# Optimization experiments

Measured on AMD Instinct MI355X. Metric: run time of the kernel, lower is better.

Reference implementation:

```python
import jax, jax.numpy as jnp
import numpy as np

D_MODEL = 1024
NUM_HEADS = 16
HEAD_DIM = D_MODEL // NUM_HEADS


def setup_inputs() -> dict:
    key = jax.random.key(0)
    k_x, k_wqkv, k_bqkv, k_wfc, k_bfc = jax.random.split(key, 5)
    scale_in = 1.0 / np.sqrt(D_MODEL)
    return {
        "x": jax.random.normal(k_x, (2, 2048, D_MODEL), dtype=jnp.float32),
        # torch nn.Linear stores weight as [out_features, in_features]
        "w_qkv": jax.random.uniform(k_wqkv, (3 * D_MODEL, D_MODEL), jnp.float32, -scale_in, scale_in),
        "b_qkv": jax.random.uniform(k_bqkv, (3 * D_MODEL,), jnp.float32, -scale_in, scale_in),
        "w_fc": jax.random.uniform(k_wfc, (D_MODEL, D_MODEL), jnp.float32, -scale_in, scale_in),
        "b_fc": jax.random.uniform(k_bfc, (D_MODEL,), jnp.float32, -scale_in, scale_in),
    }


def reference(x, w_qkv, b_qkv, w_fc, b_fc):
    B, S, _ = x.shape
    # fused QKV projection: [B,S,3*d_model]
    qkv = jnp.einsum("bsd,ed->bse", x, w_qkv) + b_qkv
    # [B,S,H,3*head_dim] -> [B,H,S,3*head_dim]
    qkv = qkv.reshape(B, S, NUM_HEADS, 3 * HEAD_DIM).transpose(0, 2, 1, 3)
    Q, K, V = jnp.split(qkv, 3, axis=-1)  # each [B,H,S,head_dim]
    scores = jnp.einsum("bhqd,bhkd->bhqk", Q, K) / np.sqrt(HEAD_DIM).astype(np.float32)
    attention = jax.nn.softmax(scores, axis=-1)  # [B,H,S,S]
    values = jnp.einsum("bhqk,bhkd->bhqd", attention, V)
    # [B,H,S,head_dim] -> [B,S,d_model]
    values = values.transpose(0, 2, 1, 3).reshape(B, S, D_MODEL)
    out = jnp.einsum("bsd,ed->bse", values, w_fc) + b_fc
    return out
```

## Files before the change

kernel.cpp:

```cpp
#include <hip/hip_runtime.h>
#include <hip/hip_bf16.h>
#include <hip/hip_fp16.h>

#define D_MODEL 1024
#define NH 16
#define HD 64
#define BATCH 2
#define SEQ 2048

typedef __attribute__((ext_vector_type(8))) short short8;
typedef __attribute__((ext_vector_type(4))) float floatx4;
typedef __attribute__((ext_vector_type(8))) _Float16 half8;

static __device__ __forceinline__ short f2bf(float f) {
    __hip_bfloat16 h = __float2bfloat16(f);
    return *reinterpret_cast<short*>(&h);
}
static __device__ __forceinline__ unsigned int pk2bf(float a, float b) {
    float2 t; t.x = a; t.y = b;
    __hip_bfloat162 h2 = __float22bfloat162_rn(t);
    return *reinterpret_cast<unsigned int*>(&h2);
}

#define GLDS(gp, lp) __builtin_amdgcn_global_load_lds( \
    (const __attribute__((address_space(1))) void*)(gp), \
    (__attribute__((address_space(3))) void*)(lp), 16, 0, 0)

__global__ __launch_bounds__(256) void cvt_all(
    const float* __restrict__ x, const float* __restrict__ wq,
    const float* __restrict__ wf,
    short* __restrict__ Xb, short* __restrict__ Wqb, short* __restrict__ Wfb)
{
    int i = blockIdx.x * 256 + threadIdx.x;
    const float* src; short* dst; int off;
    if (i < 524288)      { src = x;  dst = Xb;  off = i; }
    else if (i < 917504) { src = wq; dst = Wqb; off = i - 524288; }
    else                 { src = wf; dst = Wfb; off = i - 917504; }
    float4 a = *reinterpret_cast<const float4*>(src + off * 8);
    float4 b = *reinterpret_cast<const float4*>(src + off * 8 + 4);
    short8 o;
    o[0] = f2bf(a.x); o[1] = f2bf(a.y); o[2] = f2bf(a.z); o[3] = f2bf(a.w);
    o[4] = f2bf(b.x); o[5] = f2bf(b.y); o[6] = f2bf(b.z); o[7] = f2bf(b.w);
    *reinterpret_cast<short8*>(dst + off * 8) = o;
}

__global__ __launch_bounds__(256) void qkv_gemm(
    const short* __restrict__ X, const short* __restrict__ W,
    const float* __restrict__ bias,
    short* __restrict__ Qs, short* __restrict__ Ks, short* __restrict__ Vt_g)
{
    __shared__ __align__(16) short As[128 * 128];
    __shared__ __align__(16) short Bs[128 * 128];
    const int tid = threadIdx.x;

    const int lin = blockIdx.x;
    const int g = lin & 7;
    const int loc = lin >> 3;
    const int mi = loc / 3;
    const int j3 = loc - mi * 3;
    const int m0 = mi * 128;
    const int n0 = (g + 8 * j3) * 128;
    const int bi = m0 >> 11, sl0 = m0 & 2047;

    const int w = tid >> 6, lane = tid & 63;
    const int quad = lane >> 4, l15 = lane & 15;
    const int wm2 = w >> 1, wn2 = w & 1;

    const int rg = lane >> 3;
    const int sl = lane & 7;
    const int cg = sl ^ rg;

    floatx4 acc[4][4];
#pragma unroll
    for (int i = 0; i < 4; i++)
#pragma unroll
        for (int j = 0; j < 4; j++) acc[i][j] = (floatx4)0.0f;

    for (int k0 = 0; k0 < 1024; k0 += 128) {
        __syncthreads();
#pragma unroll
        for (int jj = 0; jj < 4; jj++) {
            int grp = w * 4 + jj;
            int r = grp * 8 + rg;
#pragma unroll
            for (int kh = 0; kh < 2; kh++) {
                GLDS(&X[(size_t)(m0 + r) * 1024 + k0 + kh * 64 + cg * 8],
                     &As[grp * 1024 + kh * 512]);
                GLDS(&W[(size_t)(n0 + r) * 1024 + k0 + kh * 64 + cg * 8],
                     &Bs[grp * 1024 + kh * 512]);
            }
        }
        __syncthreads();
#pragma unroll
        for (int kk = 0; kk < 4; kk++) {
            const int kw = kk * 32 + quad * 8;
            const int base = (kw >> 6) * 512 +
                             ((((kw & 63) >> 3) ^ (l15 & 7)) * 8);
            short8 a[4], b[4];
#pragma unroll
            for (int t = 0; t < 4; t++) {
                int ra = wm2 * 64 + t * 16 + l15;
                int rb = wn2 * 64 + t * 16 + l15;
                a[t] = *reinterpret_cast<const short8*>(
                    &As[(ra >> 3) * 1024 + (ra & 7) * 64 + base]);
                b[t] = *reinterpret_cast<const short8*>(
                    &Bs[(rb >> 3) * 1024 + (rb & 7) * 64 + base]);
            }
#pragma unroll
            for (int mt = 0; mt < 4; mt++)
#pragma unroll
                for (int nt = 0; nt < 4; nt++)
                    acc[mt][nt] = __builtin_amdgcn_mfma_f32_16x16x32_bf16(
                        a[mt], b[nt], acc[mt][nt], 0, 0, 0);
        }
    }

    __syncthreads();
    short* EA = &As[0];
    short* T  = &As[0];
#pragma unroll
    for (int half = 0; half < 2; half++) {
        const int colg0 = n0 + half * 64;
        const int h = colg0 / 192;
        const int t = (colg0 % 192) / 64;
        if (wn2 == half) {
#pragma unroll
            for (int nt = 0; nt < 4; nt++) {
                int jj = nt * 16 + l15;
                float bv = bias[colg0 + jj];
#pragma unroll
                for (int mt = 0; mt < 4; mt++) {
#pragma unroll
                    for (int r = 0; r < 4; r++) {
                        int ml = wm2 * 64 + mt * 16 + quad * 4 + r;
                        float v = acc[mt][nt][r] + bv;
                        if (t == 0) v *= 0.18033688f;
                        if (t < 2) EA[ml * 72 + jj] = f2bf(v);
                        else       T[jj * 136 + ml] = f2bf(v);
                    }
                }
            }
        }
        __syncthreads();
        if (t < 2) {
            short* dst = (t == 0) ? Qs : Ks;
#pragma unroll
            for (int i = 0; i < 4; i++) {
                int c = tid + i * 256;
                int row = c >> 3, ck = c & 7;
                uint4 u = *reinterpret_cast<const uint4*>(&EA[row * 72 + ck * 8]);
                *reinterpret_cast<uint4*>(
                    &dst[((size_t)(bi * NH + h) * SEQ + sl0 + row) * HD + ck * 8]) = u;
            }
        } else {
#pragma unroll
            for (int i = 0; i < 4; i++) {
                int c = tid + i * 256;
                int d = c >> 4, ck = c & 15;
                uint4 u = *reinterpret_cast<const uint4*>(&T[d * 136 + ck * 8]);
                *reinterpret_cast<uint4*>(
                    &Vt_g[((size_t)(bi * NH + h) * HD + d) * SEQ + sl0 + ck * 8]) = u;
            }
        }
        __syncthreads();
    }
}

__global__ __launch_bounds__(256, 2) void attn_kernel(
    const short* __restrict__ Qs, const short* __restrict__ Ks,
    const short* __restrict__ Vt_g,
    _Float16* __restrict__ Opart, float* __restrict__ lpart)
{
    __shared__ __align__(16) short Kl[64][72];
    __shared__ __align__(16) short Vt[64][72];
    __shared__ __align__(16) short Pl[4][64][72];

    const int tid = threadIdx.x;
    const int w = tid >> 6, lane = tid & 63;
    const int quad = lane >> 4, l15 = lane & 15;
    const int bx = blockIdx.x;
    const int khalf = bx & 1;
    const int q0 = (bx >> 1) * 256;
    const int h = blockIdx.y, bi = blockIdx.z;
    const int bh = bi * NH + h;
    const int kbase = bh * SEQ * HD;
    const int vbase = bh * HD * SEQ;
    const int kt0 = khalf * (SEQ / 2);

    const int kr0 = tid >> 3,         kc0 = (tid & 7) * 8;
    const int kr1 = (tid + 256) >> 3, kc1 = (tid & 7) * 8;

    const short8 onesv = {(short)0x3F80, (short)0x3F80, (short)0x3F80, (short)0x3F80,
                          (short)0x3F80, (short)0x3F80, (short)0x3F80, (short)0x3F80};

    short8 aq[4][2];
#pragma unroll
    for (int qt2 = 0; qt2 < 4; qt2++) {
        const short* qp = Qs + kbase + (q0 + w * 64 + qt2 * 16 + l15) * HD;
#pragma unroll
        for (int c = 0; c < 2; c++)
            aq[qt2][c] = *reinterpret_cast<const short8*>(qp + c * 32 + quad * 8);
    }

    floatx4 o[4][4], ol[4];
#pragma unroll
    for (int qt2 = 0; qt2 < 4; qt2++) {
        ol[qt2] = (floatx4)0.0f;
#pragma unroll
        for (int nt = 0; nt < 4; nt++) o[qt2][nt] = (floatx4)0.0f;
    }

    for (int it = 0; it < SEQ / 128; it++) {
        const int kt = kt0 + it * 64;
        __syncthreads();
        *reinterpret_cast<uint4*>(&Kl[kr0][kc0]) =
            *reinterpret_cast<const uint4*>(&Ks[kbase + (kt + kr0) * HD + kc0]);
        *reinterpret_cast<uint4*>(&Kl[kr1][kc1]) =
            *reinterpret_cast<const uint4*>(&Ks[kbase + (kt + kr1) * HD + kc1]);
        *reinterpret_cast<uint4*>(&Vt[kr0][kc0]) =
            *reinterpret_cast<const uint4*>(&Vt_g[vbase + kr0 * SEQ + kt + kc0]);
        *reinterpret_cast<uint4*>(&Vt[kr1][kc1]) =
            *reinterpret_cast<const uint4*>(&Vt_g[vbase + kr1 * SEQ + kt + kc1]);
        __syncthreads();

        short8 bk[4][2];
#pragma unroll
        for (int kt2 = 0; kt2 < 4; kt2++)
#pragma unroll
            for (int c = 0; c < 2; c++)
                bk[kt2][c] = *reinterpret_cast<const short8*>(
                    &Kl[kt2 * 16 + l15][c * 32 + quad * 8]);

#pragma unroll
        for (int qt2 = 0; qt2 < 4; qt2++) {
            floatx4 sf[4];
#pragma unroll
            for (int kt2 = 0; kt2 < 4; kt2++) sf[kt2] = (floatx4)0.0f;
#pragma unroll
            for (int c = 0; c < 2; c++)
#pragma unroll
                for (int kt2 = 0; kt2 < 4; kt2++)
                    sf[kt2] = __builtin_amdgcn_mfma_f32_16x16x32_bf16(
                        bk[kt2][c], aq[qt2][c], sf[kt2], 0, 0, 0);
#pragma unroll
            for (int kt2 = 0; kt2 < 4; kt2++) {
                uint2 p;
                p.x = pk2bf(exp2f(sf[kt2][0]), exp2f(sf[kt2][1]));
                p.y = pk2bf(exp2f(sf[kt2][2]), exp2f(sf[kt2][3]));
                *reinterpret_cast<uint2*>(
                    &Pl[w][qt2 * 16 + l15][kt2 * 16 + quad * 4]) = p;
            }
        }
        asm volatile("s_waitcnt lgkmcnt(0)" ::: "memory");

#pragma unroll
        for (int c = 0; c < 2; c++) {
            short8 vf[4];
#pragma unroll
            for (int nt = 0; nt < 4; nt++)
                vf[nt] = *reinterpret_cast<const short8*>(
                    &Vt[nt * 16 + l15][c * 32 + quad * 8]);
#pragma unroll
            for (int qt2 = 0; qt2 < 4; qt2++) {
                short8 ap = *reinterpret_cast<const short8*>(
                    &Pl[w][qt2 * 16 + l15][c * 32 + quad * 8]);
#pragma unroll
                for (int nt = 0; nt < 4; nt++)
                    o[qt2][nt] = __builtin_amdgcn_mfma_f32_16x16x32_bf16(
                        ap, vf[nt], o[qt2][nt], 0, 0, 0);
                ol[qt2] = __builtin_amdgcn_mfma_f32_16x16x32_bf16(
                    ap, onesv, ol[qt2], 0, 0, 0);
            }
        }
    }

#pragma unroll
    for (int qt2 = 0; qt2 < 4; qt2++) {
#pragma unroll
        for (int r = 0; r < 4; r++) {
            int ql = q0 + w * 64 + qt2 * 16 + quad * 4 + r;
            size_t base = (size_t)khalf * (4096u * 1024u) +
                          ((size_t)bi * SEQ + ql) * D_MODEL + h * HD;
#pragma unroll
            for (int nt = 0; nt < 4; nt++)
                Opart[base + nt * 16 + l15] = (_Float16)o[qt2][nt][r];
            if (l15 == 0)
                lpart[khalf * 65536 + bh * SEQ + ql] = ol[qt2][r];
        }
    }
}

__global__ __launch_bounds__(256) void combine_kernel(
    const _Float16* __restrict__ O, const float* __restrict__ lp,
    short* __restrict__ attnb)
{
    int i = blockIdx.x * 256 + threadIdx.x;
    int m = i >> 7;
    int e0 = (i & 127) * 8;
    int bi = m >> 11, s = m & 2047, h = e0 >> 6;
    int bh = bi * NH + h;
    float l = lp[bh * SEQ + s] + lp[65536 + bh * SEQ + s];
    float rl = 1.0f / l;
    size_t off = (size_t)m * D_MODEL + e0;
    half8 a = *reinterpret_cast<const half8*>(O + off);
    half8 b = *reinterpret_cast<const half8*>(O + 4096u * 1024u + off);
    short8 out;
#pragma unroll
    for (int j = 0; j < 8; j++)
        out[j] = f2bf(((float)a[j] + (float)b[j]) * rl);
    *reinterpret_cast<short8*>(attnb + off) = out;
}

__global__ __launch_bounds__(256) void fc_gemm(
    const short* __restrict__ A, const short* __restrict__ W,
    const float* __restrict__ bias, float* __restrict__ out)
{
    __shared__ __align__(16) short As[128 * 64];
    __shared__ __align__(16) short Bs[64 * 64];
    const int tid = threadIdx.x;
    const int m0 = blockIdx.y * 128;
    const int n0 = blockIdx.x * 64;
    const int w = tid >> 6, lane = tid & 63;
    const int quad = lane >> 4, l15 = lane & 15;
    const int wm2 = w >> 1, wn2 = w & 1;

    const int rg = lane >> 3;
    const int sl = lane & 7;
    const int cg = sl ^ rg;

    floatx4 acc[4][2];
#pragma unroll
    for (int i = 0; i < 4; i++)
#pragma unroll
        for (int j = 0; j < 2; j++) acc[i][j] = (floatx4)0.0f;

    for (int k0 = 0; k0 < 1024; k0 += 64) {
        __syncthreads();
#pragma unroll
        for (int j = 0; j < 4; j++) {
            int g = w * 4 + j;
            int r = g * 8 + rg;
            GLDS(&A[(size_t)(m0 + r) * 1024 + k0 + cg * 8], &As[g * 512]);
        }
#pragma unroll
        for (int j = 0; j < 2; j++) {
            int g = w * 2 + j;
            int r = g * 8 + rg;
            GLDS(&W[(size_t)(n0 + r) * 1024 + k0 + cg * 8], &Bs[g * 512]);
        }
        __syncthreads();
#pragma unroll
        for (int kk = 0; kk < 2; kk++) {
            int swz = ((kk * 4 + quad) ^ (l15 & 7)) * 8;
            short8 a[4], b[2];
#pragma unroll
            for (int i = 0; i < 4; i++)
                a[i] = *reinterpret_cast<const short8*>(
                    &As[(wm2 * 64 + i * 16 + l15) * 64 + swz]);
#pragma unroll
            for (int j = 0; j < 2; j++)
                b[j] = *reinterpret_cast<const short8*>(
                    &Bs[(wn2 * 32 + j * 16 + l15) * 64 + swz]);
#pragma unroll
            for (int mt = 0; mt < 4; mt++)
#pragma unroll
                for (int nt = 0; nt < 2; nt++)
                    acc[mt][nt] = __builtin_amdgcn_mfma_f32_16x16x32_bf16(
                        a[mt], b[nt], acc[mt][nt], 0, 0, 0);
        }
    }

#pragma unroll
    for (int nt = 0; nt < 2; nt++) {
        int col = n0 + wn2 * 32 + nt * 16 + l15;
        float bv = bias[col];
#pragma unroll
        for (int mt = 0; mt < 4; mt++) {
#pragma unroll
            for (int r = 0; r < 4; r++) {
                int row = m0 + wm2 * 64 + mt * 16 + quad * 4 + r;
                out[row * 1024 + col] = acc[mt][nt][r] + bv;
            }
        }
    }
}

extern "C" void kernel_launch(void* const* d_in, const int* in_sizes, int n_in,
                              void* d_out, int out_size, void* d_ws, size_t ws_size,
                              hipStream_t stream) {
    const float* x     = (const float*)d_in[0];
    const float* w_qkv = (const float*)d_in[1];
    const float* b_qkv = (const float*)d_in[2];
    const float* w_fc  = (const float*)d_in[3];
    const float* b_fc  = (const float*)d_in[4];
    float* out = (float*)d_out;

    const size_t M1 = 1024u * 1024u;
    short* ws = (short*)d_ws;
    short* Qs    = ws;
    short* Ks    = ws + 4 * M1;
    short* Vt_g  = ws + 8 * M1;
    short* Wfb   = ws + 12 * M1;
    short* Xb    = ws + 13 * M1;
    short* Wqb   = ws + 17 * M1;
    _Float16* Opart = (_Float16*)(ws + 13 * M1);
    float* lpart = (float*)(ws + 21 * M1);
    short* attnb = Qs;

    cvt_all<<<4096, 256, 0, stream>>>(x, w_qkv, w_fc, Xb, Wqb, Wfb);
    qkv_gemm<<<768, 256, 0, stream>>>(Xb, Wqb, b_qkv, Qs, Ks, Vt_g);
    attn_kernel<<<dim3(16, 16, 2), 256, 0, stream>>>(Qs, Ks, Vt_g, Opart, lpart);
    combine_kernel<<<2048, 256, 0, stream>>>(Opart, lpart, attnb);
    fc_gemm<<<dim3(16, 32), 256, 0, stream>>>(attnb, Wfb, b_fc, out);
}
```

Before: 207.8 us.

## Rewrite attention with 32x32x16 MFMA, register-resident P via permlane32 swap, no LDS

The attention kernel moves from 16x16x32 MFMA tiles with K, V and P staged through shared memory to 32x32x16 MFMA tiles. The exponentiated scores are repacked in registers with v_permlane32_swap so they can feed the PV matmul as the A operand directly. K and V fragments are loaded straight from global memory per wave, which removes all LDS traffic and __syncthreads barriers. In exchange, every wave in a block reloads the same K/V tiles through the cache hierarchy, and the larger accumulator tiles raise register pressure.

```diff
diff --git a/kernel.cpp b/kernel.cpp
--- a/kernel.cpp
+++ b/kernel.cpp
@@ -10,6 +10,7 @@
 
 typedef __attribute__((ext_vector_type(8))) short short8;
 typedef __attribute__((ext_vector_type(4))) float floatx4;
+typedef __attribute__((ext_vector_type(16))) float floatx16;
 typedef __attribute__((ext_vector_type(8))) _Float16 half8;
 
 static __device__ __forceinline__ short f2bf(float f) {
@@ -20,6 +21,15 @@
     float2 t; t.x = a; t.y = b;
     __hip_bfloat162 h2 = __float22bfloat162_rn(t);
     return *reinterpret_cast<unsigned int*>(&h2);
+}
+static __device__ __forceinline__ void pl32swap(unsigned &a, unsigned &b) {
+    asm("v_permlane32_swap_b32 %0, %1" : "+v"(a), "+v"(b));
+}
+static __device__ __forceinline__ short8 mk8(unsigned a, unsigned b,
+                                             unsigned c, unsigned d) {
+    union { unsigned u[4]; short8 s; } t;
+    t.u[0] = a; t.u[1] = b; t.u[2] = c; t.u[3] = d;
+    return t.s;
 }
 
 #define GLDS(gp, lp) __builtin_amdgcn_global_load_lds( \
@@ -171,13 +181,9 @@
     const short* __restrict__ Vt_g,
     _Float16* __restrict__ Opart, float* __restrict__ lpart)
 {
-    __shared__ __align__(16) short Kl[64][72];
-    __shared__ __align__(16) short Vt[64][72];
-    __shared__ __align__(16) short Pl[4][64][72];
-
     const int tid = threadIdx.x;
     const int w = tid >> 6, lane = tid & 63;
-    const int quad = lane >> 4, l15 = lane & 15;
+    const int hi = lane >> 5, l31 = lane & 31;
     const int bx = blockIdx.x;
     const int khalf = bx & 1;
     const int q0 = (bx >> 1) * 256;
@@ -186,106 +192,85 @@
     const int kbase = bh * SEQ * HD;
     const int vbase = bh * HD * SEQ;
     const int kt0 = khalf * (SEQ / 2);
-
-    const int kr0 = tid >> 3,         kc0 = (tid & 7) * 8;
-    const int kr1 = (tid + 256) >> 3, kc1 = (tid & 7) * 8;
+    const int qw = q0 + w * 64;
 
     const short8 onesv = {(short)0x3F80, (short)0x3F80, (short)0x3F80, (short)0x3F80,
                           (short)0x3F80, (short)0x3F80, (short)0x3F80, (short)0x3F80};
 
-    short8 aq[4][2];
-#pragma unroll
-    for (int qt2 = 0; qt2 < 4; qt2++) {
-        const short* qp = Qs + kbase + (q0 + w * 64 + qt2 * 16 + l15) * HD;
-#pragma unroll
-        for (int c = 0; c < 2; c++)
-            aq[qt2][c] = *reinterpret_cast<const short8*>(qp + c * 32 + quad * 8);
-    }
-
-    floatx4 o[4][4], ol[4];
-#pragma unroll
-    for (int qt2 = 0; qt2 < 4; qt2++) {
-        ol[qt2] = (floatx4)0.0f;
-#pragma unroll
-        for (int nt = 0; nt < 4; nt++) o[qt2][nt] = (floatx4)0.0f;
-    }
-
-    for (int it = 0; it < SEQ / 128; it++) {
-        const int kt = kt0 + it * 64;
-        __syncthreads();
-        *reinterpret_cast<uint4*>(&Kl[kr0][kc0]) =
-            *reinterpret_cast<const uint4*>(&Ks[kbase + (kt + kr0) * HD + kc0]);
-        *reinterpret_cast<uint4*>(&Kl[kr1][kc1]) =
-            *reinterpret_cast<const uint4*>(&Ks[kbase + (kt + kr1) * HD + kc1]);
-        *reinterpret_cast<uint4*>(&Vt[kr0][kc0]) =
-            *reinterpret_cast<const uint4*>(&Vt_g[vbase + kr0 * SEQ + kt + kc0]);
-        *reinterpret_cast<uint4*>(&Vt[kr1][kc1]) =
-            *reinterpret_cast<const uint4*>(&Vt_g[vbase + kr1 * SEQ + kt + kc1]);
-        __syncthreads();
-
-        short8 bk[4][2];
-#pragma unroll
-        for (int kt2 = 0; kt2 < 4; kt2++)
-#pragma unroll
-            for (int c = 0; c < 2; c++)
-                bk[kt2][c] = *reinterpret_cast<const short8*>(
-                    &Kl[kt2 * 16 + l15][c * 32 + quad * 8]);
-
-#pragma unroll
-        for (int qt2 = 0; qt2 < 4; qt2++) {
-            floatx4 sf[4];
-#pragma unroll
-            for (int kt2 = 0; kt2 < 4; kt2++) sf[kt2] = (floatx4)0.0f;
-#pragma unroll
-            for (int c = 0; c < 2; c++)
-#pragma unroll
-                for (int kt2 = 0; kt2 < 4; kt2++)
-                    sf[kt2] = __builtin_amdgcn_mfma_f32_16x16x32_bf16(
-                        bk[kt2][c], aq[qt2][c], sf[kt2], 0, 0, 0);
-#pragma unroll
-            for (int kt2 = 0; kt2 < 4; kt2++) {
-                uint2 p;
-                p.x = pk2bf(exp2f(sf[kt2][0]), exp2f(sf[kt2][1]));
-                p.y = pk2bf(exp2f(sf[kt2][2]), exp2f(sf[kt2][3]));
-                *reinterpret_cast<uint2*>(
-                    &Pl[w][qt2 * 16 + l15][kt2 * 16 + quad * 4]) = p;
-            }
-        }
-        asm volatile("s_waitcnt lgkmcnt(0)" ::: "memory");
-
-#pragma unroll
-        for (int c = 0; c < 2; c++) {
-            short8 vf[4];
-#pragma unroll
-            for (int nt = 0; nt < 4; nt++)
-                vf[nt] = *reinterpret_cast<const short8*>(
-                    &Vt[nt * 16 + l15][c * 32 + quad * 8]);
-#pragma unroll
-            for (int qt2 = 0; qt2 < 4; qt2++) {
-                short8 ap = *reinterpret_cast<const short8*>(
-                    &Pl[w][qt2 * 16 + l15][c * 32 + quad * 8]);
-#pragma unroll
-                for (int nt = 0; nt < 4; nt++)
-                    o[qt2][nt] = __builtin_amdgcn_mfma_f32_16x16x32_bf16(
-                        ap, vf[nt], o[qt2][nt], 0, 0, 0);
-                ol[qt2] = __builtin_amdgcn_mfma_f32_16x16x32_bf16(
-                    ap, onesv, ol[qt2], 0, 0, 0);
-            }
-        }
-    }
-
-#pragma unroll
-    for (int qt2 = 0; qt2 < 4; qt2++) {
-#pragma unroll
-        for (int r = 0; r < 4; r++) {
-            int ql = q0 + w * 64 + qt2 * 16 + quad * 4 + r;
+    short8 aq[2][4];
+#pragma unroll
+    for (int qt = 0; qt < 2; qt++) {
+        const short* qp = Qs + kbase + (size_t)(qw + qt * 32 + l31) * HD + hi * 8;
+#pragma unroll
+        for (int c = 0; c < 4; c++)
+            aq[qt][c] = *reinterpret_cast<const short8*>(qp + c * 16);
+    }
+
+    floatx16 o[2][2], ol[2];
+#pragma unroll
+    for (int qt = 0; qt < 2; qt++) {
+        ol[qt] = (floatx16)0.0f;
+        o[qt][0] = (floatx16)0.0f;
+        o[qt][1] = (floatx16)0.0f;
+    }
+
+#pragma unroll 2
+    for (int it = 0; it < SEQ / 2 / 32; it++) {
+        const int kt = kt0 + it * 32;
+        const short* kp = Ks + kbase + (size_t)(kt + l31) * HD + hi * 8;
+        short8 kf0 = *reinterpret_cast<const short8*>(kp);
+        short8 kf1 = *reinterpret_cast<const short8*>(kp + 16);
+        short8 kf2 = *reinterpret_cast<const short8*>(kp + 32);
+        short8 kf3 = *reinterpret_cast<const short8*>(kp + 48);
+        const short* vp = Vt_g + vbase + (size_t)l31 * SEQ + kt + hi * 8;
+        short8 vf00 = *reinterpret_cast<const short8*>(vp);
+        short8 vf10 = *reinterpret_cast<const short8*>(vp + 16);
+        short8 vf01 = *reinterpret_cast<const short8*>(vp + 32 * SEQ);
+        short8 vf11 = *reinterpret_cast<const short8*>(vp + 32 * SEQ + 16);
+
+#pragma unroll
+        for (int qt = 0; qt < 2; qt++) {
+            floatx16 s = (floatx16)0.0f;
+            s = __builtin_amdgcn_mfma_f32_32x32x16_bf16(kf0, aq[qt][0], s, 0, 0, 0);
+            s = __builtin_amdgcn_mfma_f32_32x32x16_bf16(kf1, aq[qt][1], s, 0, 0, 0);
+            s = __builtin_amdgcn_mfma_f32_32x32x16_bf16(kf2, aq[qt][2], s, 0, 0, 0);
+            s = __builtin_amdgcn_mfma_f32_32x32x16_bf16(kf3, aq[qt][3], s, 0, 0, 0);
+
+            float p[16];
+#pragma unroll
+            for (int r = 0; r < 16; r++) p[r] = exp2f(s[r]);
+
+            unsigned d0a = pk2bf(p[0], p[1]),   d2a = pk2bf(p[4], p[5]);
+            unsigned d1a = pk2bf(p[2], p[3]),   d3a = pk2bf(p[6], p[7]);
+            pl32swap(d0a, d2a);
+            pl32swap(d1a, d3a);
+            unsigned d0b = pk2bf(p[8], p[9]),   d2b = pk2bf(p[12], p[13]);
+            unsigned d1b = pk2bf(p[10], p[11]), d3b = pk2bf(p[14], p[15]);
+            pl32swap(d0b, d2b);
+            pl32swap(d1b, d3b);
+            short8 pa0 = mk8(d0a, d1a, d2a, d3a);
+            short8 pa1 = mk8(d0b, d1b, d2b, d3b);
+
+            o[qt][0] = __builtin_amdgcn_mfma_f32_32x32x16_bf16(pa0, vf00, o[qt][0], 0, 0, 0);
+            o[qt][1] = __builtin_amdgcn_mfma_f32_32x32x16_bf16(pa0, vf01, o[qt][1], 0, 0, 0);
+            o[qt][0] = __builtin_amdgcn_mfma_f32_32x32x16_bf16(pa1, vf10, o[qt][0], 0, 0, 0);
+            o[qt][1] = __builtin_amdgcn_mfma_f32_32x32x16_bf16(pa1, vf11, o[qt][1], 0, 0, 0);
+            ol[qt] = __builtin_amdgcn_mfma_f32_32x32x16_bf16(pa0, onesv, ol[qt], 0, 0, 0);
+            ol[qt] = __builtin_amdgcn_mfma_f32_32x32x16_bf16(pa1, onesv, ol[qt], 0, 0, 0);
+        }
+    }
+
+#pragma unroll
+    for (int qt = 0; qt < 2; qt++) {
+#pragma unroll
+        for (int r = 0; r < 16; r++) {
+            int ql = qw + qt * 32 + (r & 3) + 8 * (r >> 2) + 4 * hi;
             size_t base = (size_t)khalf * (4096u * 1024u) +
                           ((size_t)bi * SEQ + ql) * D_MODEL + h * HD;
-#pragma unroll
-            for (int nt = 0; nt < 4; nt++)
-                Opart[base + nt * 16 + l15] = (_Float16)o[qt2][nt][r];
-            if (l15 == 0)
-                lpart[khalf * 65536 + bh * SEQ + ql] = ol[qt2][r];
+            Opart[base + l31]      = (_Float16)o[qt][0][r];
+            Opart[base + 32 + l31] = (_Float16)o[qt][1][r];
+            if (l31 == 0)
+                lpart[khalf * 65536 + bh * SEQ + ql] = ol[qt][r];
         }
     }
 }
```

Measured after the change: 218.7 us. 1.05x slower.
